# Optimization experiments

Measured on AMD Instinct MI355X. Metric: run time of the kernel, lower is better.

The kernel has to match this reference:

```python
import jax, jax.numpy as jnp
import numpy as np
import math

DIM, NH, HD = 4096, 32, 128
B, S = 2, 2048
MAX_SEQ, INIT_SLICE = 4096, 2048  # init_slice = max_seq_len - max_prompt_size
NEG = -1e9


def setup_inputs() -> dict:
    key = jax.random.key(0)
    ks = jax.random.split(key, 6)
    x = jax.random.normal(ks[0], (B, S, DIM), dtype=jnp.float32)
    scale = 1.0 / math.sqrt(DIM)
    wq = jax.random.normal(ks[1], (DIM, DIM), dtype=jnp.float32) * scale
    wk = jax.random.normal(ks[2], (DIM, DIM), dtype=jnp.float32) * scale
    wv = jax.random.normal(ks[3], (DIM, DIM), dtype=jnp.float32) * scale
    wo = jax.random.normal(ks[4], (DIM, DIM), dtype=jnp.float32) * scale
    # RoPE frequencies, viewed as real pairs [S, HD//2, 2] = (cos, sin)
    inv_freq = 1.0 / (10000.0 ** (jnp.arange(0, HD, 2, dtype=jnp.float32) / HD))
    ang = jnp.arange(S, dtype=jnp.float32)[:, None] * inv_freq[None, :]  # [S, HD//2]
    freqs_cis_real = jnp.stack([jnp.cos(ang), jnp.sin(ang)], axis=-1)
    # causal additive mask [1,1,S,S]
    mask = jnp.where(jnp.triu(jnp.ones((S, S), dtype=bool), k=1), NEG, 0.0)[None, None].astype(jnp.float32)
    cache_k = jnp.zeros((B, MAX_SEQ, NH, HD), dtype=jnp.float32)
    cache_v = jnp.zeros((B, MAX_SEQ, NH, HD), dtype=jnp.float32)
    return {"x": x, "freqs_cis_real": freqs_cis_real, "mask": mask,
            "wq": wq, "wk": wk, "wv": wv, "wo": wo,
            "cache_k": cache_k, "cache_v": cache_v, "slice_size": 2048}


def _apply_rotary(xq, xk, freqs_cis_real):
    # xq, xk: [b, s, h, d]; pairs along last dim are (real, imag)
    b, s, h, d = xq.shape
    fr = freqs_cis_real[None, :, None, :, 0]  # [1, s, 1, d//2]
    fi = freqs_cis_real[None, :, None, :, 1]

    def rot(t):
        t = t.reshape(b, s, h, d // 2, 2)
        tr, ti = t[..., 0], t[..., 1]
        out = jnp.stack([tr * fr - ti * fi, tr * fi + ti * fr], axis=-1)
        return out.reshape(b, s, h, d)

    return rot(xq), rot(xk)


def reference(x, freqs_cis_real, mask, wq, wk, wv, wo, cache_k, cache_v, slice_size):
    bsz, seqlen, _ = x.shape
    xq = (x @ wq.T).reshape(bsz, seqlen, NH, HD)
    xk = (x @ wk.T).reshape(bsz, seqlen, NH, HD)
    xv = (x @ wv.T).reshape(bsz, seqlen, NH, HD)
    xq, xk = _apply_rotary(xq, xk, freqs_cis_real)
    # prompt-phase (seqlen > 1) cache update: cat(cache[:, :init_slice], new)
    cache_k_new = jnp.concatenate([cache_k[:bsz, :INIT_SLICE], xk], axis=1)
    cache_v_new = jnp.concatenate([cache_v[:bsz, :INIT_SLICE], xv], axis=1)
    keys = cache_k_new[:, -slice_size:]    # [b, k, h, d]
    values = cache_v_new[:, -slice_size:]
    scores = jnp.einsum('bqhd,bkhd->bhqk', xq, keys) / math.sqrt(HD)
    scores = scores + mask
    probs = jax.nn.softmax(scores.astype(jnp.float32), axis=-1).astype(xq.dtype)
    out = jnp.einsum('bhqk,bkhd->bqhd', probs, values).reshape(bsz, seqlen, -1)
    return out @ wo.T
```

## Files before the change

### kernel.cpp

```cpp
#include <hip/hip_runtime.h>
#include <hip/hip_bf16.h>
#include <stdint.h>

#define SEQ   2048
#define NHEAD 32
#define HDIM  128
#define DMODEL 4096
#define MTOT  4096
#define RSCALE 0.08838834764831845f

typedef __hip_bfloat16 bf16_t;
typedef __attribute__((ext_vector_type(8))) short short8v;
typedef __attribute__((ext_vector_type(4))) short short4v;
typedef __attribute__((ext_vector_type(4))) float f32x4;

typedef __attribute__((address_space(3))) void lds_void;
typedef __attribute__((address_space(1))) void gbl_void;
#define TO_LDS(p) ((lds_void*)(uint32_t)(uintptr_t)(p))
#define TO_GBL(p) ((gbl_void*)(uintptr_t)(p))
#define ASYNC_CP16(g, l) __builtin_amdgcn_global_load_lds(TO_GBL(g), TO_LDS(l), 16, 0, 0)

__device__ __forceinline__ float bf2f(short u) {
  union { uint32_t i; float f; } x; x.i = ((uint32_t)(uint16_t)u) << 16; return x.f;
}

__global__ __launch_bounds__(256) void cast_f32_to_bf16(const float* __restrict__ in,
                                                        bf16_t* __restrict__ out) {
  size_t i = (size_t)blockIdx.x * 256 + threadIdx.x;
  const f32x4* p = (const f32x4*)in + i * 2;
  f32x4 a = p[0], b = p[1];
  __align__(16) bf16_t tmp[8];
#pragma unroll
  for (int j = 0; j < 4; ++j) tmp[j]     = __float2bfloat16(a[j]);
#pragma unroll
  for (int j = 0; j < 4; ++j) tmp[4 + j] = __float2bfloat16(b[j]);
  *(short8v*)(out + i * 8) = *(const short8v*)tmp;
}

#define VMW_(N) asm volatile("s_waitcnt vmcnt(" #N ")" ::: "memory")
#define VMW(N) VMW_(N)

#define STAGE_A(mh_, X)                                                        \
  { const int tr_ = tid >> 3, c_ = tid & 7;                                    \
    _Pragma("unroll")                                                          \
    for (int i_ = 0; i_ < 2; ++i_) {                                           \
      const int row_ = (mh_) * 64 + i_ * 128 + tr_;                            \
      const int cg_ = c_ ^ (row_ & 7);                                         \
      ASYNC_CP16(gA0 + (size_t)row_ * 4096 + (size_t)(X) * 64 + cg_ * 8,       \
                 ldsc + (((X) & 1) << 16) + row_ * 128 + c_ * 16); } }

#define STAGE_B(nh_, X)                                                        \
  { const int tr_ = tid >> 3, c_ = tid & 7;                                    \
    _Pragma("unroll")                                                          \
    for (int i_ = 0; i_ < 2; ++i_) {                                           \
      const int row_ = i_ * 128 + (tr_ >> 5) * 64 + (nh_) * 32 + (tr_ & 31);   \
      const int cg_ = c_ ^ (row_ & 7);                                         \
      ASYNC_CP16(gB0 + (size_t)row_ * 4096 + (size_t)(X) * 64 + cg_ * 8,       \
                 ldsc + (((X) & 1) << 16) + 32768 + row_ * 128 + c_ * 16); } }

#define TILE4(T, DOSTG, VA, VB, VC)                                            \
  {                                                                            \
    const int sb = ((T) & 1) << 16;                                            \
    const int Xn = (T) + 1;                                                    \
    short8v a0[4][2], a1[4][2], b0[2][2], b1[2][2];                            \
                                                 \
    VMW(VA);                                                                   \
    __builtin_amdgcn_s_barrier();                                              \
    __builtin_amdgcn_sched_barrier(0);                                         \
    _Pragma("unroll") for (int m = 0; m < 4; ++m)                              \
      _Pragma("unroll") for (int kk = 0; kk < 2; ++kk)                         \
        a0[m][kk] = *(const short8v*)(ldsc + sb + aRow + m * 2048 + (kk ? cx1 : cx0)); \
    _Pragma("unroll") for (int n = 0; n < 2; ++n)                              \
      _Pragma("unroll") for (int kk = 0; kk < 2; ++kk)                         \
        b0[n][kk] = *(const short8v*)(ldsc + sb + bRow + n * 2048 + (kk ? cx1 : cx0)); \
    if (DOSTG) STAGE_A(0, Xn);                                                 \
    asm volatile("s_waitcnt lgkmcnt(0)" ::: "memory");                         \
    __builtin_amdgcn_sched_barrier(0);                                         \
    __builtin_amdgcn_s_setprio(1);                                             \
    _Pragma("unroll") for (int m = 0; m < 4; ++m)                              \
      _Pragma("unroll") for (int n = 0; n < 2; ++n)                            \
        _Pragma("unroll") for (int kk = 0; kk < 2; ++kk)                       \
          acc[m][n] = __builtin_amdgcn_mfma_f32_16x16x32_bf16(a0[m][kk], b0[n][kk], acc[m][n], 0, 0, 0); \
    __builtin_amdgcn_s_setprio(0);                                             \
                                                 \
    VMW(VB);                                                                   \
    __builtin_amdgcn_s_barrier();                                              \
    __builtin_amdgcn_sched_barrier(0);                                         \
    _Pragma("unroll") for (int n = 0; n < 2; ++n)                              \
      _Pragma("unroll") for (int kk = 0; kk < 2; ++kk)                         \
        b1[n][kk] = *(const short8v*)(ldsc + sb + bRow + 4096 + n * 2048 + (kk ? cx1 : cx0)); \
    if (DOSTG) STAGE_B(0, Xn);                                                 \
    asm volatile("s_waitcnt lgkmcnt(0)" ::: "memory");                         \
    __builtin_amdgcn_sched_barrier(0);                                         \
    __builtin_amdgcn_s_setprio(1);                                             \
    _Pragma("unroll") for (int m = 0; m < 4; ++m)                              \
      _Pragma("unroll") for (int n = 0; n < 2; ++n)                            \
        _Pragma("unroll") for (int kk = 0; kk < 2; ++kk)                       \
          acc[m][2 + n] = __builtin_amdgcn_mfma_f32_16x16x32_bf16(a0[m][kk], b1[n][kk], acc[m][2 + n], 0, 0, 0); \
    __builtin_amdgcn_s_setprio(0);                                             \
                                                 \
    VMW(VC);                                                                   \
    __builtin_amdgcn_s_barrier();                                              \
    __builtin_amdgcn_sched_barrier(0);                                         \
    _Pragma("unroll") for (int m = 0; m < 4; ++m)                              \
      _Pragma("unroll") for (int kk = 0; kk < 2; ++kk)                         \
        a1[m][kk] = *(const short8v*)(ldsc + sb + aRow + 8192 + m * 2048 + (kk ? cx1 : cx0)); \
    if (DOSTG) STAGE_B(1, Xn);                                                 \
    asm volatile("s_waitcnt lgkmcnt(0)" ::: "memory");                         \
    __builtin_amdgcn_sched_barrier(0);                                         \
    __builtin_amdgcn_s_setprio(1);                                             \
    _Pragma("unroll") for (int m = 0; m < 4; ++m)                              \
      _Pragma("unroll") for (int n = 0; n < 2; ++n)                            \
        _Pragma("unroll") for (int kk = 0; kk < 2; ++kk)                       \
          acc[4 + m][2 + n] = __builtin_amdgcn_mfma_f32_16x16x32_bf16(a1[m][kk], b1[n][kk], acc[4 + m][2 + n], 0, 0, 0); \
    __builtin_amdgcn_s_setprio(0);                                             \
     \
    if (DOSTG) STAGE_A(1, Xn);                                                 \
    __builtin_amdgcn_s_setprio(1);                                             \
    _Pragma("unroll") for (int m = 0; m < 4; ++m)                              \
      _Pragma("unroll") for (int n = 0; n < 2; ++n)                            \
        _Pragma("unroll") for (int kk = 0; kk < 2; ++kk)                       \
          acc[4 + m][n] = __builtin_amdgcn_mfma_f32_16x16x32_bf16(a1[m][kk], b0[n][kk], acc[4 + m][n], 0, 0, 0); \
    __builtin_amdgcn_s_setprio(0);                                             \
  }

template <bool OUT_BF16>
__global__ __launch_bounds__(512, 2) void gemm_nt(const bf16_t* __restrict__ A,
                                                  const bf16_t* __restrict__ B0,
                                                  const bf16_t* __restrict__ B1,
                                                  const bf16_t* __restrict__ B2,
                                                  void* __restrict__ Cout) {
  __shared__ __align__(16) char ldsbuf[131072];
  char* ldsc = ldsbuf;
  const int z = blockIdx.z;
  const bf16_t* __restrict__ Bm = (z == 0) ? B0 : (z == 1 ? B1 : B2);
  const int tid = threadIdx.x;
  const int wave = tid >> 6, lane = tid & 63;
  const int bid = blockIdx.x;
  const int xcd = bid & 7, idx = bid >> 3;
  const int bm = xcd * 2 + (idx >> 4);
  const int bn = idx & 15;
  const int wr = wave >> 2, wc = wave & 3;
  const int r = lane & 15, g = lane >> 4;

  f32x4 acc[8][4] = {};

  const bf16_t* gA0 = A  + (size_t)bm * 256 * 4096;
  const bf16_t* gB0 = Bm + (size_t)bn * 256 * 4096;

  const int swz = r & 7;
  const int cx0 = (g ^ swz) << 4;
  const int cx1 = ((4 + g) ^ swz) << 4;
  const int aRow = (wr * 128 + r) * 128;
  const int bRow = 32768 + (wc * 64 + r) * 128;

  STAGE_A(0, 0);
  STAGE_B(0, 0);
  STAGE_B(1, 0);
  STAGE_A(1, 0);

  for (int T = 0; T < 63; ++T) TILE4(T, 1, 4, 4, 4);
  TILE4(63, 0, 4, 2, 0);

  const size_t row_base = (size_t)bm * 256 + wr * 128 + g * 4;
  const size_t col_base = (size_t)bn * 256 + wc * 64 + r;
  if (OUT_BF16) {
    bf16_t* C = (bf16_t*)Cout + (size_t)z * 16777216u;
#pragma unroll
    for (int m = 0; m < 8; ++m)
#pragma unroll
      for (int n = 0; n < 4; ++n)
#pragma unroll
        for (int j = 0; j < 4; ++j)
          C[(row_base + m * 16 + j) * 4096 + col_base + n * 16] = __float2bfloat16(acc[m][n][j]);
  } else {
    float* C = (float*)Cout;
#pragma unroll
    for (int m = 0; m < 8; ++m)
#pragma unroll
      for (int n = 0; n < 4; ++n)
#pragma unroll
        for (int j = 0; j < 4; ++j)
          C[(row_base + m * 16 + j) * 4096 + col_base + n * 16] = acc[m][n][j];
  }
}

__global__ __launch_bounds__(256) void rope_kernel(const bf16_t* __restrict__ qkv,
                                                   const float* __restrict__ freqs,
                                                   bf16_t* __restrict__ qrot,
                                                   bf16_t* __restrict__ krot) {
  const int which = blockIdx.y;
  const bf16_t* __restrict__ src = qkv + (size_t)which * 16777216u;
  bf16_t* __restrict__ dst = (which == 0) ? qrot : krot;
  const float sc = (which == 0) ? RSCALE : 1.0f;
  size_t t = (size_t)blockIdx.x * 256 + threadIdx.x;
  int dg = t & 15;
  int s  = (int)(t >> 4) & 2047;
  int bh = (int)(t >> 15);
  int b  = bh >> 5;
  int d0 = dg * 8;

  short8v v = *(const short8v*)&src[((size_t)(b * 2048 + s)) * 4096 + (bh & 31) * 128 + d0];
  const float* fp = freqs + (size_t)s * 128 + d0;
  f32x4 f0 = *(const f32x4*)fp;
  f32x4 f1 = *(const f32x4*)(fp + 4);
  float fr[4] = {f0[0], f0[2], f1[0], f1[2]};
  float fi[4] = {f0[1], f0[3], f1[1], f1[3]};
  __align__(16) bf16_t tmp[8];
#pragma unroll
  for (int i = 0; i < 4; ++i) {
    float tr = bf2f(v[2 * i]), ti = bf2f(v[2 * i + 1]);
    tmp[2 * i]     = __float2bfloat16((tr * fr[i] - ti * fi[i]) * sc);
    tmp[2 * i + 1] = __float2bfloat16((tr * fi[i] + ti * fr[i]) * sc);
  }
  *(short8v*)&dst[((size_t)bh * 2048 + s) * 128 + d0] = *(const short8v*)tmp;
}

__global__ __launch_bounds__(256) void vtrans_kernel(const bf16_t* __restrict__ xv,
                                                     bf16_t* __restrict__ vt) {
  __shared__ bf16_t tile[64 * 136];
  const int s0 = blockIdx.x * 64;
  const int bh = blockIdx.y;
  const int b = bh >> 5, h = bh & 31;
  const int tid = threadIdx.x;
#pragma unroll
  for (int it = 0; it < 4; ++it) {
    int c = it * 256 + tid;
    int row = c >> 4, col8 = c & 15;
    short8v v = *(const short8v*)&xv[((size_t)(b * 2048 + s0 + row)) * 4096 + h * 128 + col8 * 8];
    *(short8v*)&tile[row * 136 + col8 * 8] = v;
  }
  __syncthreads();
#pragma unroll
  for (int it = 0; it < 4; ++it) {
    int c = it * 256 + tid;
    int d = c >> 3, sc = c & 7;
    __align__(16) bf16_t tmp[8];
#pragma unroll
    for (int i = 0; i < 8; ++i) tmp[i] = tile[(sc * 8 + i) * 136 + d];
    *(short8v*)&vt[((size_t)(bh * 128 + d)) * 2048 + s0 + sc * 8] = *(const short8v*)tmp;
  }
}

#define PSTR 72
__global__ __launch_bounds__(512) void attn_kernel(const bf16_t* __restrict__ qrot,
                                                   const bf16_t* __restrict__ krot,
                                                   const bf16_t* __restrict__ vt,
                                                   bf16_t* __restrict__ att) {
  __shared__ bf16_t Kls[64 * 128];
  __shared__ bf16_t Vls[128 * 64];
  __shared__ bf16_t Pls[8][16 * PSTR];

  const int lid  = blockIdx.x;
  const int xcd  = lid & 7;
  const int kk_  = lid >> 3;
  const int bh   = xcd + 8 * ((kk_ >> 4) & 7);
  const int qidx = 15 - (kk_ & 15);
  const int warp = threadIdx.x >> 6;
  const int lane = threadIdx.x & 63;
  const int r = lane & 15, g = lane >> 4;

  const bf16_t* __restrict__ Q  = qrot + (size_t)bh * 2048 * 128;
  const bf16_t* __restrict__ Kp = krot + (size_t)bh * 2048 * 128;
  const bf16_t* __restrict__ Vt = vt   + (size_t)bh * 128 * 2048;
  bf16_t* __restrict__ Pw = &Pls[warp][0];

  const int qB = qidx * 128 + warp * 16;
  const int ntiles = 2 * qidx + 2;

  short8v qf[4];
#pragma unroll
  for (int kk = 0; kk < 4; ++kk)
    qf[kk] = *(const short8v*)&Q[(size_t)(qB + r) * 128 + kk * 32 + g * 8];

  float l = 0.f;
  f32x4 o[8];
#pragma unroll
  for (int n2 = 0; n2 < 8; ++n2) o[n2] = f32x4{0.f, 0.f, 0.f, 0.f};

  const int rA = lane >> 4, cA = lane & 15;
  const int rB = lane >> 3, cB = lane & 7;
  const int swz = (r & 7) << 4;

  for (int t = 0; t < ntiles; ++t) {
    const int kb = t * 64;

#pragma unroll
    for (int i = 0; i < 2; ++i) {
      const int krow = warp * 8 + i * 4 + rA;
      const int kcol = 8 * (cA ^ ((i * 4 + rA) & 7));
      ASYNC_CP16(Kp + (size_t)(kb + krow) * 128 + kcol,
                 (char*)Kls + (size_t)(krow * 128 + cA * 8) * 2);
    }
#pragma unroll
    for (int i = 0; i < 2; ++i) {
      const int vrow = warp * 16 + i * 8 + rB;
      const int vcol = 8 * (cB ^ rB);
      ASYNC_CP16(Vt + (size_t)vrow * 2048 + kb + vcol,
                 (char*)Vls + (size_t)(vrow * 64 + cB * 8) * 2);
    }
    __syncthreads();

    if (kb <= qB + 15) {
      f32x4 sacc[4];
#pragma unroll
      for (int n = 0; n < 4; ++n) sacc[n] = f32x4{0.f, 0.f, 0.f, 0.f};
#pragma unroll
      for (int n = 0; n < 4; ++n)
#pragma unroll
        for (int kk = 0; kk < 4; ++kk) {
          short8v kf = *(const short8v*)((const char*)Kls +
                         (n * 16 + r) * 256 + ((kk * 64 + g * 16) ^ swz));
          sacc[n] = __builtin_amdgcn_mfma_f32_16x16x32_bf16(kf, qf[kk], sacc[n], 0, 0, 0);
        }

      float p[16];
#pragma unroll
      for (int n = 0; n < 4; ++n)
#pragma unroll
        for (int j = 0; j < 4; ++j)
          p[n * 4 + j] = __expf(sacc[n][j]);

      if (kb + 63 > qB) {
        const int qa = qB + r;
#pragma unroll
        for (int n = 0; n < 4; ++n)
#pragma unroll
          for (int j = 0; j < 4; ++j)
            if (kb + n * 16 + g * 4 + j > qa) p[n * 4 + j] = 0.f;
      }

      {
        float ts[8];
#pragma unroll
        for (int i = 0; i < 8; ++i) ts[i] = p[i] + p[i + 8];
#pragma unroll
        for (int i = 0; i < 4; ++i) ts[i] += ts[i + 4];
        float rs = (ts[0] + ts[1]) + (ts[2] + ts[3]);
        rs += __shfl_xor(rs, 16, 64);
        rs += __shfl_xor(rs, 32, 64);
        l += rs;
      }

#pragma unroll
      for (int n = 0; n < 4; ++n) {
        __align__(8) bf16_t tp[4];
#pragma unroll
        for (int j = 0; j < 4; ++j) tp[j] = __float2bfloat16(p[n * 4 + j]);
        *(short4v*)&Pw[r * PSTR + n * 16 + g * 4] = *(const short4v*)tp;
      }

#pragma unroll
      for (int kk2 = 0; kk2 < 2; ++kk2) {
        short8v pf = *(const short8v*)&Pw[r * PSTR + kk2 * 32 + g * 8];
#pragma unroll
        for (int n2 = 0; n2 < 8; ++n2) {
          short8v vf = *(const short8v*)((const char*)Vls +
                         (n2 * 16 + r) * 128 + ((kk2 * 64 + g * 16) ^ swz));
          o[n2] = __builtin_amdgcn_mfma_f32_16x16x32_bf16(pf, vf, o[n2], 0, 0, 0);
        }
      }
    }
    __syncthreads();
  }

  float lq[4];
#pragma unroll
  for (int j = 0; j < 4; ++j) lq[j] = 1.0f / __shfl(l, g * 4 + j, 64);
  const int b = bh >> 5, h = bh & 31;
#pragma unroll
  for (int n2 = 0; n2 < 8; ++n2)
#pragma unroll
    for (int j = 0; j < 4; ++j)
      att[((size_t)(b * 2048 + qB + g * 4 + j)) * 4096 + h * 128 + n2 * 16 + r] =
          __float2bfloat16(o[n2][j] * lq[j]);
}

extern "C" void kernel_launch(void* const* d_in, const int* in_sizes, int n_in,
                              void* d_out, int out_size, void* d_ws, size_t ws_size,
                              hipStream_t stream) {
  (void)in_sizes; (void)n_in; (void)out_size; (void)ws_size;
  const float* x  = (const float*)d_in[0];
  const float* fr = (const float*)d_in[1];
  const float* wq = (const float*)d_in[3];
  const float* wk = (const float*)d_in[4];
  const float* wv = (const float*)d_in[5];
  const float* wo = (const float*)d_in[6];

  char* ws = (char*)d_ws;
  const size_t MB32 = 33554432;
  bf16_t* xb  = (bf16_t*)(ws + 0 * MB32);
  bf16_t* wqb = (bf16_t*)(ws + 1 * MB32);
  bf16_t* wkb = (bf16_t*)(ws + 2 * MB32);
  bf16_t* wvb = (bf16_t*)(ws + 3 * MB32);
  bf16_t* qkv = (bf16_t*)(ws + 4 * MB32);

  cast_f32_to_bf16<<<8192, 256, 0, stream>>>(x,  xb);
  cast_f32_to_bf16<<<8192, 256, 0, stream>>>(wq, wqb);
  cast_f32_to_bf16<<<8192, 256, 0, stream>>>(wk, wkb);
  cast_f32_to_bf16<<<8192, 256, 0, stream>>>(wv, wvb);

  gemm_nt<true><<<dim3(256, 1, 3), 512, 0, stream>>>(xb, wqb, wkb, wvb, (void*)qkv);

  bf16_t* qrot = xb;
  bf16_t* krot = wqb;
  bf16_t* vtp  = wkb;
  bf16_t* attb = wvb;

  rope_kernel<<<dim3(8192, 2), 256, 0, stream>>>(qkv, fr, qrot, krot);
  vtrans_kernel<<<dim3(32, 64), 256, 0, stream>>>(qkv + 2 * 16777216u, vtp);

  bf16_t* wob = qkv;
  cast_f32_to_bf16<<<8192, 256, 0, stream>>>(wo, wob);

  attn_kernel<<<1024, 512, 0, stream>>>(qrot, krot, vtp, attb);

  gemm_nt<false><<<dim3(256, 1, 1), 512, 0, stream>>>(attb, wob, wob, wob, d_out);
}
```

Baseline: 666.6 us.

## Triple-buffer attention K/V loads, reorder GEMM staging, remap tiles, fuse casts

```diff
diff --git a/kernel.cpp b/kernel.cpp
--- a/kernel.cpp
+++ b/kernel.cpp
@@ -24,6 +24,25 @@
   union { uint32_t i; float f; } x; x.i = ((uint32_t)(uint16_t)u) << 16; return x.f;
 }
 
+__global__ __launch_bounds__(256) void cast4_f32_to_bf16(const float* __restrict__ s0,
+                                                         const float* __restrict__ s1,
+                                                         const float* __restrict__ s2,
+                                                         const float* __restrict__ s3,
+                                                         bf16_t* __restrict__ out) {
+  const int w = blockIdx.y;
+  const float* in = (w == 0) ? s0 : ((w == 1) ? s1 : ((w == 2) ? s2 : s3));
+  bf16_t* o = out + (size_t)w * 16777216u;
+  size_t i = (size_t)blockIdx.x * 256 + threadIdx.x;
+  const f32x4* p = (const f32x4*)in + i * 2;
+  f32x4 a = p[0], b = p[1];
+  __align__(16) bf16_t tmp[8];
+#pragma unroll
+  for (int j = 0; j < 4; ++j) tmp[j]     = __float2bfloat16(a[j]);
+#pragma unroll
+  for (int j = 0; j < 4; ++j) tmp[4 + j] = __float2bfloat16(b[j]);
+  *(short8v*)(o + i * 8) = *(const short8v*)tmp;
+}
+
 __global__ __launch_bounds__(256) void cast_f32_to_bf16(const float* __restrict__ in,
                                                         bf16_t* __restrict__ out) {
   size_t i = (size_t)blockIdx.x * 256 + threadIdx.x;
@@ -39,6 +58,7 @@
 
 #define VMW_(N) asm volatile("s_waitcnt vmcnt(" #N ")" ::: "memory")
 #define VMW(N) VMW_(N)
+#define SB0 __builtin_amdgcn_sched_barrier(0)
 
 #define STAGE_A(mh_, X)                                                        \
   { const int tr_ = tid >> 3, c_ = tid & 7;                                    \
@@ -66,16 +86,15 @@
                                                  \
     VMW(VA);                                                                   \
     __builtin_amdgcn_s_barrier();                                              \
-    __builtin_amdgcn_sched_barrier(0);                                         \
+    SB0;                                                                       \
+    if (DOSTG) STAGE_A(0, Xn);                                                 \
+    SB0;                                                                       \
     _Pragma("unroll") for (int m = 0; m < 4; ++m)                              \
       _Pragma("unroll") for (int kk = 0; kk < 2; ++kk)                         \
         a0[m][kk] = *(const short8v*)(ldsc + sb + aRow + m * 2048 + (kk ? cx1 : cx0)); \
     _Pragma("unroll") for (int n = 0; n < 2; ++n)                              \
       _Pragma("unroll") for (int kk = 0; kk < 2; ++kk)                         \
         b0[n][kk] = *(const short8v*)(ldsc + sb + bRow + n * 2048 + (kk ? cx1 : cx0)); \
-    if (DOSTG) STAGE_A(0, Xn);                                                 \
-    asm volatile("s_waitcnt lgkmcnt(0)" ::: "memory");                         \
-    __builtin_amdgcn_sched_barrier(0);                                         \
     __builtin_amdgcn_s_setprio(1);                                             \
     _Pragma("unroll") for (int m = 0; m < 4; ++m)                              \
       _Pragma("unroll") for (int n = 0; n < 2; ++n)                            \
@@ -85,13 +104,12 @@
                                                  \
     VMW(VB);                                                                   \
     __builtin_amdgcn_s_barrier();                                              \
-    __builtin_amdgcn_sched_barrier(0);                                         \
+    SB0;                                                                       \
+    if (DOSTG) STAGE_B(0, Xn);                                                 \
+    SB0;                                                                       \
     _Pragma("unroll") for (int n = 0; n < 2; ++n)                              \
       _Pragma("unroll") for (int kk = 0; kk < 2; ++kk)                         \
         b1[n][kk] = *(const short8v*)(ldsc + sb + bRow + 4096 + n * 2048 + (kk ? cx1 : cx0)); \
-    if (DOSTG) STAGE_B(0, Xn);                                                 \
-    asm volatile("s_waitcnt lgkmcnt(0)" ::: "memory");                         \
-    __builtin_amdgcn_sched_barrier(0);                                         \
     __builtin_amdgcn_s_setprio(1);                                             \
     _Pragma("unroll") for (int m = 0; m < 4; ++m)                              \
       _Pragma("unroll") for (int n = 0; n < 2; ++n)                            \
@@ -101,20 +119,19 @@
                                                  \
     VMW(VC);                                                                   \
     __builtin_amdgcn_s_barrier();                                              \
-    __builtin_amdgcn_sched_barrier(0);                                         \
+    SB0;                                                                       \
+    if (DOSTG) STAGE_B(1, Xn);                                                 \
+    SB0;                                                                       \
     _Pragma("unroll") for (int m = 0; m < 4; ++m)                              \
       _Pragma("unroll") for (int kk = 0; kk < 2; ++kk)                         \
         a1[m][kk] = *(const short8v*)(ldsc + sb + aRow + 8192 + m * 2048 + (kk ? cx1 : cx0)); \
-    if (DOSTG) STAGE_B(1, Xn);                                                 \
-    asm volatile("s_waitcnt lgkmcnt(0)" ::: "memory");                         \
-    __builtin_amdgcn_sched_barrier(0);                                         \
     __builtin_amdgcn_s_setprio(1);                                             \
     _Pragma("unroll") for (int m = 0; m < 4; ++m)                              \
       _Pragma("unroll") for (int n = 0; n < 2; ++n)                            \
         _Pragma("unroll") for (int kk = 0; kk < 2; ++kk)                       \
           acc[4 + m][2 + n] = __builtin_amdgcn_mfma_f32_16x16x32_bf16(a1[m][kk], b1[n][kk], acc[4 + m][2 + n], 0, 0, 0); \
     __builtin_amdgcn_s_setprio(0);                                             \
-     \
+                                     \
     if (DOSTG) STAGE_A(1, Xn);                                                 \
     __builtin_amdgcn_s_setprio(1);                                             \
     _Pragma("unroll") for (int m = 0; m < 4; ++m)                              \
@@ -138,8 +155,8 @@
   const int wave = tid >> 6, lane = tid & 63;
   const int bid = blockIdx.x;
   const int xcd = bid & 7, idx = bid >> 3;
-  const int bm = xcd * 2 + (idx >> 4);
-  const int bn = idx & 15;
+  const int bm = (xcd >> 1) * 4 + (idx >> 3);
+  const int bn = (xcd & 1) * 8 + (idx & 7);
   const int wr = wave >> 2, wc = wave & 3;
   const int r = lane & 15, g = lane >> 4;
 
@@ -247,8 +264,8 @@
                                                    const bf16_t* __restrict__ krot,
                                                    const bf16_t* __restrict__ vt,
                                                    bf16_t* __restrict__ att) {
-  __shared__ bf16_t Kls[64 * 128];
-  __shared__ bf16_t Vls[128 * 64];
+  __shared__ bf16_t Kls[3][64 * 128];
+  __shared__ bf16_t Vls[3][128 * 64];
   __shared__ bf16_t Pls[8][16 * PSTR];
 
   const int lid  = blockIdx.x;
@@ -282,26 +299,40 @@
   const int rB = lane >> 3, cB = lane & 7;
   const int swz = (r & 7) << 4;
 
-  for (int t = 0; t < ntiles; ++t) {
-    const int kb = t * 64;
-
+  auto STG = [&](int kb_, int buf) {
 #pragma unroll
     for (int i = 0; i < 2; ++i) {
       const int krow = warp * 8 + i * 4 + rA;
-      const int kcol = 8 * (cA ^ ((i * 4 + rA) & 7));
-      ASYNC_CP16(Kp + (size_t)(kb + krow) * 128 + kcol,
-                 (char*)Kls + (size_t)(krow * 128 + cA * 8) * 2);
+      const int kcol = 8 * (cA ^ (krow & 7));
+      ASYNC_CP16(Kp + (size_t)(kb_ + krow) * 128 + kcol,
+                 (char*)&Kls[buf][0] + (size_t)(krow * 128 + cA * 8) * 2);
     }
 #pragma unroll
     for (int i = 0; i < 2; ++i) {
       const int vrow = warp * 16 + i * 8 + rB;
       const int vcol = 8 * (cB ^ rB);
-      ASYNC_CP16(Vt + (size_t)vrow * 2048 + kb + vcol,
-                 (char*)Vls + (size_t)(vrow * 64 + cB * 8) * 2);
+      ASYNC_CP16(Vt + (size_t)vrow * 2048 + kb_ + vcol,
+                 (char*)&Vls[buf][0] + (size_t)(vrow * 64 + cB * 8) * 2);
     }
-    __syncthreads();
+  };
+
+  STG(0, 0);
+  int cur = 0;
+  for (int t = 0; t < ntiles; ++t) {
+    const int kb = t * 64;
+    const int nxt = (cur == 2) ? 0 : cur + 1;
+    if (t + 1 < ntiles) {
+      STG(kb + 64, nxt);
+      VMW(4);
+    } else {
+      VMW(0);
+    }
+    __builtin_amdgcn_s_barrier();
+    SB0;
 
     if (kb <= qB + 15) {
+      const char* Kc = (const char*)&Kls[cur][0];
+      const char* Vc = (const char*)&Vls[cur][0];
       f32x4 sacc[4];
 #pragma unroll
       for (int n = 0; n < 4; ++n) sacc[n] = f32x4{0.f, 0.f, 0.f, 0.f};
@@ -309,8 +340,7 @@
       for (int n = 0; n < 4; ++n)
 #pragma unroll
         for (int kk = 0; kk < 4; ++kk) {
-          short8v kf = *(const short8v*)((const char*)Kls +
-                         (n * 16 + r) * 256 + ((kk * 64 + g * 16) ^ swz));
+          short8v kf = *(const short8v*)(Kc + (n * 16 + r) * 256 + ((kk * 64 + g * 16) ^ swz));
           sacc[n] = __builtin_amdgcn_mfma_f32_16x16x32_bf16(kf, qf[kk], sacc[n], 0, 0, 0);
         }
 
@@ -355,13 +385,12 @@
         short8v pf = *(const short8v*)&Pw[r * PSTR + kk2 * 32 + g * 8];
 #pragma unroll
         for (int n2 = 0; n2 < 8; ++n2) {
-          short8v vf = *(const short8v*)((const char*)Vls +
-                         (n2 * 16 + r) * 128 + ((kk2 * 64 + g * 16) ^ swz));
+          short8v vf = *(const short8v*)(Vc + (n2 * 16 + r) * 128 + ((kk2 * 64 + g * 16) ^ swz));
           o[n2] = __builtin_amdgcn_mfma_f32_16x16x32_bf16(pf, vf, o[n2], 0, 0, 0);
         }
       }
     }
-    __syncthreads();
+    cur = nxt;
   }
 
   float lq[4];
@@ -395,10 +424,7 @@
   bf16_t* wvb = (bf16_t*)(ws + 3 * MB32);
   bf16_t* qkv = (bf16_t*)(ws + 4 * MB32);
 
-  cast_f32_to_bf16<<<8192, 256, 0, stream>>>(x,  xb);
-  cast_f32_to_bf16<<<8192, 256, 0, stream>>>(wq, wqb);
-  cast_f32_to_bf16<<<8192, 256, 0, stream>>>(wk, wkb);
-  cast_f32_to_bf16<<<8192, 256, 0, stream>>>(wv, wvb);
+  cast4_f32_to_bf16<<<dim3(8192, 4), 256, 0, stream>>>(x, wq, wk, wv, xb);
 
   gemm_nt<true><<<dim3(256, 1, 3), 512, 0, stream>>>(xb, wqb, wkb, wvb, (void*)qkv);
 
```

Measured after the change: 676.9 us. About the same (+1.6%).
